# Performance work log

Measured on AMD Instinct MI355X. Metric: run time of the kernel, lower is better.

Reference implementation:

```python
import jax, jax.numpy as jnp
import numpy as np

D = 64            # node_out_feats
G = 1000          # number of graphs in batch
NPG = 32          # nodes per graph
N = G * NPG       # total nodes = 32000
E = 80000         # total edges
NODE_IN = 74
EDGE_IN = 12
EH = 128          # edge_hidden_feats
STEPS_MP = 6
STEPS_S2S = 6
LSTM_LAYERS = 3
N_TASKS = 1


def setup_inputs() -> dict:
    key = jax.random.key(0)
    ks = jax.random.split(key, 32)

    def lin(k, fi, fo):
        return (jax.random.normal(k, (fi, fo), jnp.float32) / np.float32(np.sqrt(fi)))

    # edges constrained within graphs
    eg = jax.random.randint(ks[0], (E,), 0, G)
    inp = {
        "node_feats": jax.random.normal(ks[1], (N, NODE_IN), jnp.float32),
        "edge_feats": jax.random.normal(ks[2], (E, EDGE_IN), jnp.float32),
        "src": (eg * NPG + jax.random.randint(ks[3], (E,), 0, NPG)).astype(jnp.int32),
        "dst": (eg * NPG + jax.random.randint(ks[4], (E,), 0, NPG)).astype(jnp.int32),
        "segment_ids": (jnp.arange(N, dtype=jnp.int32) // NPG),
        "Wp": lin(ks[5], NODE_IN, D), "bp": jnp.zeros((D,), jnp.float32),
        "We1": lin(ks[6], EDGE_IN, EH), "be1": jnp.zeros((EH,), jnp.float32),
        "We2": lin(ks[7], EH, D * D), "be2": jnp.zeros((D * D,), jnp.float32),
        "b_conv": jnp.zeros((D,), jnp.float32),
        "gru_Wx": lin(ks[8], D, 3 * D), "gru_Wh": lin(ks[9], D, 3 * D),
        "gru_bx": jnp.zeros((3 * D,), jnp.float32), "gru_bh": jnp.zeros((3 * D,), jnp.float32),
        "Wout1": lin(ks[10], 2 * D, D), "bout1": jnp.zeros((D,), jnp.float32),
        "Wout2": lin(ks[11], D, N_TASKS), "bout2": jnp.zeros((N_TASKS,), jnp.float32),
    }
    for l in range(LSTM_LAYERS):
        fi = 2 * D if l == 0 else D
        inp[f"lstm_Wx{l}"] = lin(ks[12 + 4 * l], fi, 4 * D)
        inp[f"lstm_Wh{l}"] = lin(ks[13 + 4 * l], D, 4 * D)
        inp[f"lstm_bx{l}"] = jnp.zeros((4 * D,), jnp.float32)
        inp[f"lstm_bh{l}"] = jnp.zeros((4 * D,), jnp.float32)
    return inp


def reference(node_feats, edge_feats, src, dst, segment_ids,
              Wp, bp, We1, be1, We2, be2, b_conv,
              gru_Wx, gru_Wh, gru_bx, gru_bh,
              Wout1, bout1, Wout2, bout2,
              lstm_Wx0, lstm_Wh0, lstm_bx0, lstm_bh0,
              lstm_Wx1, lstm_Wh1, lstm_bx1, lstm_bh1,
              lstm_Wx2, lstm_Wh2, lstm_bx2, lstm_bh2):
    # ---- MPNNGNN ----
    h = jax.nn.relu(node_feats @ Wp + bp)                 # [N, D]
    hidden = h                                            # GRU hidden state
    # edge network -> per-edge [D, D] weight matrix (edge feats are constant,
    # so compute once; DGL recomputes each step with identical result)
    W_edge = (jax.nn.relu(edge_feats @ We1 + be1) @ We2 + be2).reshape(E, D, D)
    for _ in range(STEPS_MP):
        msg = jnp.einsum('ed,edo->eo', h[src], W_edge)    # [E, D] per-edge matvec
        agg = jax.ops.segment_sum(msg, dst, num_segments=N) + b_conv
        x = jax.nn.relu(agg)
        # GRU cell (torch gate order r, z, n)
        gx = x @ gru_Wx + gru_bx
        gh = hidden @ gru_Wh + gru_bh
        r = jax.nn.sigmoid(gx[:, :D] + gh[:, :D])
        z = jax.nn.sigmoid(gx[:, D:2 * D] + gh[:, D:2 * D])
        n = jnp.tanh(gx[:, 2 * D:] + r * gh[:, 2 * D:])
        hidden = (1.0 - z) * n + z * hidden
        h = hidden
    # ---- Set2Set readout ----
    lstm = [(lstm_Wx0, lstm_Wh0, lstm_bx0, lstm_bh0),
            (lstm_Wx1, lstm_Wh1, lstm_bx1, lstm_bh1),
            (lstm_Wx2, lstm_Wh2, lstm_bx2, lstm_bh2)]
    hs = [jnp.zeros((G, D), h.dtype) for _ in range(LSTM_LAYERS)]
    cs = [jnp.zeros((G, D), h.dtype) for _ in range(LSTM_LAYERS)]
    q_star = jnp.zeros((G, 2 * D), h.dtype)
    for _ in range(STEPS_S2S):
        xq = q_star
        for l, (Wx, Wh, bx, bh) in enumerate(lstm):
            gates = xq @ Wx + bx + hs[l] @ Wh + bh        # [G, 4D], torch order i,f,g,o
            i, f, g_, o = jnp.split(gates, 4, axis=-1)
            c = jax.nn.sigmoid(f) * cs[l] + jax.nn.sigmoid(i) * jnp.tanh(g_)
            hs[l] = jax.nn.sigmoid(o) * jnp.tanh(c)
            cs[l] = c
            xq = hs[l]
        q = xq                                            # [G, D]
        e = jnp.sum(h * q[segment_ids], axis=-1)          # [N] attention logits
        emax = jax.ops.segment_max(e, segment_ids, num_segments=G)
        ee = jnp.exp(e - emax[segment_ids])
        alpha = ee / jax.ops.segment_sum(ee, segment_ids, num_segments=G)[segment_ids]
        readout = jax.ops.segment_sum(h * alpha[:, None], segment_ids, num_segments=G)
        q_star = jnp.concatenate([q, readout], axis=-1)   # [G, 2D]
    # ---- prediction head ----
    pred = jax.nn.relu(q_star @ Wout1 + bout1) @ Wout2 + bout2
    return pred, q_star
```

## Files before the change

### kernel.cpp

```cpp
#include <hip/hip_runtime.h>

typedef __attribute__((ext_vector_type(8))) _Float16 f16x8;
typedef __attribute__((ext_vector_type(4))) float floatx4;

union HFrag { uint4 u4; f16x8 v; unsigned short s[8]; };
union HS { _Float16 h; unsigned short u; };

__device__ __forceinline__ float bf2f(unsigned short u) {
  return __uint_as_float(((unsigned int)u) << 16);
}
__device__ __forceinline__ float h2f(unsigned short u) { HS z; z.u = u; return (float)z.h; }
__device__ __forceinline__ unsigned short f2h(float f) { HS z; z.h = (_Float16)f; return z.u; }
__device__ __forceinline__ float sigmf(float x) { return 1.0f / (1.0f + expf(-x)); }

__device__ __forceinline__ float ldi(const void* p, long i, bool f32) {
  return f32 ? ((const float*)p)[i] : bf2f(((const unsigned short*)p)[i]);
}

__device__ __forceinline__ void dma16(unsigned short* lds, const unsigned short* g) {
  __builtin_amdgcn_global_load_lds(
      (const __attribute__((address_space(1))) unsigned int*)g,
      (__attribute__((address_space(3))) unsigned int*)lds,
      16, 0, 0);
}

#define WAIT_VM8()   __builtin_amdgcn_s_waitcnt(0x0F78)
#define WAIT_VM4()   __builtin_amdgcn_s_waitcnt(0x0F74)
#define WAIT_VM0()   __builtin_amdgcn_s_waitcnt(0x0F70)
#define WAIT_LGKM0() __builtin_amdgcn_s_waitcnt(0xC07F)

#define NNODES 32000
#define NEDGES 80000
#define NGRAPH 1000

#define MFMA_F16 __builtin_amdgcn_mfma_f32_16x16x32_f16

__global__ __launch_bounds__(256) void detect_kernel(
    const unsigned short* __restrict__ nf, int* __restrict__ flag) {
  __shared__ float sm[256];
  float m = 0.f;
  for (int i = threadIdx.x; i < 4096; i += 256) {
    float v = fabsf(bf2f(nf[i]));
    if (isfinite(v)) m = fmaxf(m, v);
    else m = 1e30f;
  }
  sm[threadIdx.x] = m;
  __syncthreads();
  if (threadIdx.x == 0) {
    float mm = 0.f;
    for (int i = 0; i < 256; ++i) mm = fmaxf(mm, sm[i]);
    flag[0] = (mm > 1e6f) ? 1 : 0;
  }
}

__global__ __launch_bounds__(256) void prep_kernel(
    const int* __restrict__ dflag,
    const void* __restrict__ Wx, const void* __restrict__ Wh,
    const void* __restrict__ bx, const void* __restrict__ bh,
    const void* __restrict__ bconv,
    unsigned short* __restrict__ WxH, unsigned short* __restrict__ WhH,
    float* __restrict__ bxf, float* __restrict__ bhf, float* __restrict__ bconvf) {
  bool f32 = dflag[0] != 0;
  int idx = blockIdx.x * 256 + threadIdx.x;
  int j = idx >> 6, k = idx & 63;
  WxH[idx] = f2h(ldi(Wx, k * 192 + j, f32));
  WhH[idx] = f2h(ldi(Wh, k * 192 + j, f32));
  if (idx < 192) { bxf[idx] = ldi(bx, idx, f32); bhf[idx] = ldi(bh, idx, f32); }
  if (idx < 64) bconvf[idx] = ldi(bconv, idx, f32);
}

__global__ __launch_bounds__(256) void lstmprep_kernel(
    const int* __restrict__ dflag,
    const void* Wx0, const void* Wh0, const void* bx0, const void* bh0,
    const void* Wx1, const void* Wh1, const void* bx1, const void* bh1,
    const void* Wx2, const void* Wh2, const void* bx2, const void* bh2,
    float4* __restrict__ LW, float* __restrict__ bsum) {
  bool f32 = dflag[0] != 0;
  int idx = blockIdx.x * 256 + threadIdx.x;
  int l, base, fi;
  if (idx < 12288)      { l = 0; base = 0;     fi = 128; }
  else if (idx < 20480) { l = 1; base = 12288; fi = 64; }
  else                  { l = 2; base = 20480; fi = 64; }
  const void* Wx = (l == 0) ? Wx0 : (l == 1) ? Wx1 : Wx2;
  const void* Wh = (l == 0) ? Wh0 : (l == 1) ? Wh1 : Wh2;
  int r = idx - base;
  int c = r >> 8, t = r & 255;
  float v[4];
#pragma unroll
  for (int i2 = 0; i2 < 4; ++i2) {
    int k = c * 4 + i2;
    v[i2] = (k < fi) ? ldi(Wx, (long)k * 256 + t, f32)
                     : ldi(Wh, (long)(k - fi) * 256 + t, f32);
  }
  float4 o; o.x = v[0]; o.y = v[1]; o.z = v[2]; o.w = v[3];
  LW[idx] = o;
  if (idx < 768) {
    int ll = idx >> 8, j = idx & 255;
    const void* bx = (ll == 0) ? bx0 : (ll == 1) ? bx1 : bx2;
    const void* bh = (ll == 0) ? bh0 : (ll == 1) ? bh1 : bh2;
    bsum[idx] = ldi(bx, j, f32) + ldi(bh, j, f32);
  }
}

__global__ __launch_bounds__(256) void nodeproj_kernel(
    const int* __restrict__ dflag,
    const void* __restrict__ nf, const void* __restrict__ Wp,
    const void* __restrict__ bp, float* __restrict__ hstate) {
  bool f32 = dflag[0] != 0;
  int lane = threadIdx.x & 63;
  int n = blockIdx.x * 4 + (threadIdx.x >> 6);
  float acc = ldi(bp, lane, f32);
  for (int k = 0; k < 74; ++k)
    acc += ldi(nf, (long)n * 74 + k, f32) * ldi(Wp, k * 64 + lane, f32);
  hstate[n * 64 + lane] = fmaxf(acc, 0.0f);
}

__global__ __launch_bounds__(256) void we2h_kernel(
    const int* __restrict__ dflag,
    const void* __restrict__ We2, unsigned short* __restrict__ We2Hsw) {
  bool f32 = dflag[0] != 0;
  int idx = blockIdx.x * 256 + threadIdx.x;
  int j = idx & 7;
  int cc = (idx >> 3) & 15;
  int o = (idx >> 7) & 63;
  int d = idx >> 13;
  int k = ((cc ^ (o & 15)) << 3) | j;
  We2Hsw[idx] = f2h(ldi(We2, (long)k * 4096 + d * 64 + o, f32));
}

__global__ __launch_bounds__(256) void count_kernel(
    const int* __restrict__ dst, int* __restrict__ cnt) {
  int e = blockIdx.x * 256 + threadIdx.x;
  if (e < NEDGES) atomicAdd(&cnt[dst[e]], 1);
}

__global__ __launch_bounds__(256) void scan_kernel(
    const int* __restrict__ cnt, int* __restrict__ row_ptr, int* __restrict__ cur) {
  __shared__ int part[256];
  int t = threadIdx.x;
  int base = t * 125;
  int s = 0;
  for (int i = 0; i < 125; ++i) s += cnt[base + i];
  part[t] = s;
  __syncthreads();
  if (t == 0) {
    int run = 0;
    for (int i = 0; i < 256; ++i) { int v = part[i]; part[i] = run; run += v; }
  }
  __syncthreads();
  int run = part[t];
  for (int i = 0; i < 125; ++i) {
    row_ptr[base + i] = run;
    cur[base + i] = run;
    run += cnt[base + i];
  }
  if (t == 255) row_ptr[32000] = run;
}

__global__ __launch_bounds__(256) void fill_kernel(
    const int* __restrict__ dst, int* __restrict__ cur, int* __restrict__ eidx) {
  int e = blockIdx.x * 256 + threadIdx.x;
  if (e < NEDGES) { int p = atomicAdd(&cur[dst[e]], 1); eidx[p] = e; }
}

__global__ __launch_bounds__(256, 2) void msg_fused_kernel(
    const int* __restrict__ dflag,
    const float* __restrict__ hstate,
    const void* __restrict__ ef, const void* __restrict__ We1,
    const void* __restrict__ be1, const void* __restrict__ be2,
    const unsigned short* __restrict__ We2Hsw,
    const int* __restrict__ src, const int* __restrict__ eidx,
    float* __restrict__ msgbuf) {
  bool f32 = dflag[0] != 0;
  __shared__ __align__(16) unsigned short u_s[64][136];
  __shared__ float h_s[64][65];
  __shared__ __align__(8) unsigned short be2h[64][72];
  __shared__ int ssrc[64];
  __shared__ int seidx[64];
  __shared__ __align__(16) unsigned short wbuf[2][8192];
  float* ef_s = (float*)&wbuf[0][0];
  float* we1_s = (float*)&wbuf[0][2048];
  float* be1_s = (float*)&wbuf[1][0];

  int t = threadIdx.x;
  int e0 = blockIdx.x * 64;
  int lane = t & 63, w = t >> 6;

  if (t < 64) { int e = eidx[e0 + t]; seidx[t] = e; ssrc[t] = src[e]; }
  for (int i = t; i < 1536; i += 256) we1_s[i] = ldi(We1, i, f32);
  if (t < 128) be1_s[t] = ldi(be1, t, f32);
  for (int i = t; i < 4096; i += 256) be2h[i >> 6][i & 63] = f2h(ldi(be2, i, f32));
  __syncthreads();
  for (int i = t; i < 768; i += 256) {
    int slot = i / 12, k = i - slot * 12;
    ef_s[i] = ldi(ef, (long)seidx[slot] * 12 + k, f32);
  }
  __syncthreads();

#pragma unroll
  for (int i = 0; i < 32; ++i) {
    int idx = t + i * 256;
    int row = idx >> 7, col = idx & 127;
    float acc = be1_s[col];
#pragma unroll
    for (int k = 0; k < 12; ++k) acc += ef_s[row * 12 + k] * we1_s[k * 128 + col];
    u_s[row][col] = f2h(fmaxf(acc, 0.f));
  }
#pragma unroll
  for (int i = 0; i < 16; ++i) {
    int idx = t + i * 256;
    int row = idx >> 6, col = idx & 63;
    h_s[row][col] = hstate[(size_t)ssrc[row] * 64 + col];
  }
  __syncthreads();

  int o0 = w * 16;
  int c = lane & 15, q = lane >> 4;
  HFrag ub[4][4];
#pragma unroll
  for (int g = 0; g < 4; ++g)
#pragma unroll
    for (int kk = 0; kk < 4; ++kk)
      ub[g][kk].u4 = *(const uint4*)&u_s[g * 16 + c][q * 8 + kk * 32];
  floatx4 msg[4];
#pragma unroll
  for (int g = 0; g < 4; ++g) msg[g] = (floatx4){0.f, 0.f, 0.f, 0.f};
  int rowb = (o0 + c) * 16;

  unsigned short* buf0 = &wbuf[0][0];
  unsigned short* buf1 = &wbuf[1][0];
  unsigned short* buf2 = &u_s[0][0];

  {
    const unsigned short* g0 = We2Hsw + w * 2048 + lane * 8;
    unsigned short* l0 = buf0 + w * 2048;
    dma16(l0, g0); dma16(l0 + 512, g0 + 512);
    dma16(l0 + 1024, g0 + 1024); dma16(l0 + 1536, g0 + 1536);
    const unsigned short* g1 = g0 + 8192;
    unsigned short* l1 = buf1 + w * 2048;
    dma16(l1, g1); dma16(l1 + 512, g1 + 512);
    dma16(l1 + 1024, g1 + 1024); dma16(l1 + 1536, g1 + 1536);
  }
  __syncthreads();
  {
    const unsigned short* g2 = We2Hsw + 2 * 8192 + w * 2048 + lane * 8;
    unsigned short* l2 = buf2 + w * 2048;
    dma16(l2, g2); dma16(l2 + 512, g2 + 512);
    dma16(l2 + 1024, g2 + 1024); dma16(l2 + 1536, g2 + 1536);
  }

  int m3 = 0;
  for (int d = 0; d < 64; ++d) {
    if (d <= 61) WAIT_VM8();
    else if (d == 62) WAIT_VM4();
    else WAIT_VM0();
    unsigned short* wb = (m3 == 0) ? buf0 : (m3 == 1) ? buf1 : buf2;
    HFrag a0, a1, a2, a3;
    a0.u4 = *(const uint4*)&wb[(rowb + ((0 * 4 + q) ^ c)) * 8];
    a1.u4 = *(const uint4*)&wb[(rowb + ((1 * 4 + q) ^ c)) * 8];
    a2.u4 = *(const uint4*)&wb[(rowb + ((2 * 4 + q) ^ c)) * 8];
    a3.u4 = *(const uint4*)&wb[(rowb + ((3 * 4 + q) ^ c)) * 8];
    WAIT_LGKM0();
    if (d + 3 < 64) {
      const unsigned short* g = We2Hsw + (d + 3) * 8192 + w * 2048 + lane * 8;
      unsigned short* l = wb + w * 2048;
      dma16(l, g); dma16(l + 512, g + 512);
      dma16(l + 1024, g + 1024); dma16(l + 1536, g + 1536);
    }
    HS b0, b1, b2v, b3;
    const unsigned short* bp = &be2h[d][o0 + q * 4];
    b0.u = bp[0]; b1.u = bp[1]; b2v.u = bp[2]; b3.u = bp[3];
    float be0 = (float)b0.h, be1v = (float)b1.h, be2f = (float)b2v.h, be3 = (float)b3.h;
#pragma unroll
    for (int g = 0; g < 4; ++g) {
      floatx4 wv = {0.f, 0.f, 0.f, 0.f};
      wv = MFMA_F16(a0.v, ub[g][0].v, wv, 0, 0, 0);
      wv = MFMA_F16(a1.v, ub[g][1].v, wv, 0, 0, 0);
      wv = MFMA_F16(a2.v, ub[g][2].v, wv, 0, 0, 0);
      wv = MFMA_F16(a3.v, ub[g][3].v, wv, 0, 0, 0);
      float hv = h_s[g * 16 + c][d];
      msg[g][0] += hv * (wv[0] + be0);
      msg[g][1] += hv * (wv[1] + be1v);
      msg[g][2] += hv * (wv[2] + be2f);
      msg[g][3] += hv * (wv[3] + be3);
    }
    m3 = (m3 == 2) ? 0 : m3 + 1;
  }

#pragma unroll
  for (int g = 0; g < 4; ++g) {
    int slot = g * 16 + c;
    float4 st;
    st.x = msg[g][0]; st.y = msg[g][1]; st.z = msg[g][2]; st.w = msg[g][3];
    *(float4*)(msgbuf + (size_t)(e0 + slot) * 64 + o0 + q * 4) = st;
  }
}

__global__ __launch_bounds__(256, 2) void gru_kernel(
    float* __restrict__ hstate, const float* __restrict__ msgbuf,
    const int* __restrict__ row_ptr,
    const unsigned short* __restrict__ WxH, const unsigned short* __restrict__ WhH,
    const float* __restrict__ bxf, const float* __restrict__ bhf,
    const float* __restrict__ bconvf) {
  __shared__ __align__(16) unsigned short Xhi[64][72];
  __shared__ __align__(16) unsigned short Xlo[64][72];
  __shared__ __align__(16) unsigned short Hh[64][72];
  __shared__ unsigned short SRZ[128][68];
  __shared__ float GXn[64][66];
  __shared__ float GHn[64][66];
  int t = threadIdx.x;
  int nb = blockIdx.x * 64;

#pragma unroll
  for (int i = 0; i < 16; ++i) {
    int idx = t + i * 256;
    int n = idx >> 6, c = idx & 63;
    int node = nb + n;
    float a = bconvf[c];
    int p0 = row_ptr[node], p1 = row_ptr[node + 1];
    for (int p = p0; p < p1; ++p) a += msgbuf[(size_t)p * 64 + c];
    a = fmaxf(a, 0.f);
    HS hi; hi.h = (_Float16)a;
    Xhi[n][c] = hi.u;
    Xlo[n][c] = f2h(a - (float)hi.h);
    Hh[n][c] = f2h(hstate[(size_t)node * 64 + c]);
  }
  __syncthreads();

  int lane = t & 63, w = t >> 6;
  int c16 = lane & 15, q = lane >> 4;
  floatx4 gx[3][4], gh[3][4];
#pragma unroll
  for (int jt = 0; jt < 3; ++jt)
#pragma unroll
    for (int nt = 0; nt < 4; ++nt) {
      gx[jt][nt] = (floatx4){0.f, 0.f, 0.f, 0.f};
      gh[jt][nt] = (floatx4){0.f, 0.f, 0.f, 0.f};
    }
#pragma unroll
  for (int kc = 0; kc < 2; ++kc) {
    int kof = kc * 32 + q * 8;
    HFrag ax[3], ah[3];
#pragma unroll
    for (int jt = 0; jt < 3; ++jt) {
      long off = (long)((w * 3 + jt) * 16 + c16) * 64 + kof;
      ax[jt].u4 = *(const uint4*)(WxH + off);
      ah[jt].u4 = *(const uint4*)(WhH + off);
    }
    HFrag bxh[4], bxl[4], bhf_[4];
#pragma unroll
    for (int nt = 0; nt < 4; ++nt) {
      int n = nt * 16 + c16;
      bxh[nt].u4 = *(const uint4*)&Xhi[n][kof];
      bxl[nt].u4 = *(const uint4*)&Xlo[n][kof];
      bhf_[nt].u4 = *(const uint4*)&Hh[n][kof];
    }
#pragma unroll
    for (int jt = 0; jt < 3; ++jt)
#pragma unroll
      for (int nt = 0; nt < 4; ++nt) {
        gx[jt][nt] = MFMA_F16(ax[jt].v, bxh[nt].v, gx[jt][nt], 0, 0, 0);
        gx[jt][nt] = MFMA_F16(ax[jt].v, bxl[nt].v, gx[jt][nt], 0, 0, 0);
        gh[jt][nt] = MFMA_F16(ah[jt].v, bhf_[nt].v, gh[jt][nt], 0, 0, 0);
      }
  }

#pragma unroll
  for (int jt = 0; jt < 3; ++jt) {
#pragma unroll
    for (int rr = 0; rr < 4; ++rr) {
      int j = (w * 3 + jt) * 16 + q * 4 + rr;
      float bxv = bxf[j], bhv = bhf[j];
#pragma unroll
      for (int nt = 0; nt < 4; ++nt) {
        int n = nt * 16 + c16;
        float vx = gx[jt][nt][rr] + bxv;
        float vh = gh[jt][nt][rr] + bhv;
        if (j < 128) {
          SRZ[j][n] = f2h(sigmf(vx + vh));
        } else {
          GXn[j - 128][n] = vx;
          GHn[j - 128][n] = vh;
        }
      }
    }
  }
  __syncthreads();

#pragma unroll
  for (int i = 0; i < 16; ++i) {
    int idx = t + i * 256;
    int n = idx >> 6, f = idx & 63;
    float r = h2f(SRZ[f][n]);
    float z = h2f(SRZ[64 + f][n]);
    float ng = tanhf(GXn[f][n] + r * GHn[f][n]);
    size_t gi = (size_t)(nb + n) * 64 + f;
    float ho = hstate[gi];
    hstate[gi] = (1.0f - z) * ng + z * ho;
  }
}

__global__ __launch_bounds__(512) void s2s6_kernel(
    const int* __restrict__ dflag,
    const float* __restrict__ hstate,
    const float4* __restrict__ LW,
    const float* __restrict__ lstm_bsum,
    const void* __restrict__ Wout1, const void* __restrict__ bout1,
    const void* __restrict__ Wout2, const void* __restrict__ bout2,
    float* __restrict__ out) {
  bool f32 = dflag[0] != 0;
  __shared__ float xq[4][128];
  __shared__ float inb[4][192];
  __shared__ float gates[4][256];
  __shared__ float al[4][32];
  __shared__ float hsvf[768];
  __shared__ float csvf[768];
  int g0 = blockIdx.x * 4;
  int t = threadIdx.x;

  for (int i = t; i < 512; i += 512) xq[i >> 7][i & 127] = 0.f;
  for (int i = t; i < 768; i += 512) { hsvf[i] = 0.f; csvf[i] = 0.f; }
  __syncthreads();

  int tt = t & 255, gp = t >> 8;
  int ga = gp * 2, gb = ga + 1;

  for (int s = 0; s < 6; ++s) {
#pragma unroll
    for (int l = 0; l < 3; ++l) {
      const int fi = (l == 0) ? 128 : 64;
      const int tot = fi + 64;
      for (int i = t; i < 4 * tot; i += 512) {
        int g = i / tot, k = i - g * tot;
        inb[g][k] = (k < fi) ? xq[g][k] : hsvf[l * 256 + g * 64 + (k - fi)];
      }
      __syncthreads();
      const int nch = tot >> 2;
      const float4* wrow = LW + ((l == 0) ? 0 : (l == 1) ? 12288 : 20480) + tt;
      float bs = lstm_bsum[l * 256 + tt];
      float a0 = bs, a1 = bs;
#pragma unroll 8
      for (int cch = 0; cch < nch; ++cch) {
        float4 wv = wrow[(size_t)cch * 256];
        float4 x0 = *(const float4*)&inb[ga][cch * 4];
        float4 x1 = *(const float4*)&inb[gb][cch * 4];
        a0 += wv.x * x0.x + wv.y * x0.y + wv.z * x0.z + wv.w * x0.w;
        a1 += wv.x * x1.x + wv.y * x1.y + wv.z * x1.z + wv.w * x1.w;
      }
      gates[ga][tt] = a0;
      gates[gb][tt] = a1;
      __syncthreads();
      if (t < 256) {
        int gg = t >> 6, u = t & 63;
        float ig = sigmf(gates[gg][u]);
        float fg = sigmf(gates[gg][64 + u]);
        float gv = tanhf(gates[gg][128 + u]);
        float og = sigmf(gates[gg][192 + u]);
        int ci = l * 256 + t;
        float cc = fg * csvf[ci] + ig * gv;
        float hn = og * tanhf(cc);
        csvf[ci] = cc;
        hsvf[ci] = hn;
        xq[gg][u] = hn;
      }
      __syncthreads();
    }
    if (t < 256) {
      int gg = t >> 6, tl = t & 63;
      int g = g0 + gg;
      int n = tl & 31, half = tl >> 5;
      const float* hrow = hstate + (size_t)(g * 32 + n) * 64 + half * 32;
      const float* qp = &xq[gg][half * 32];
      float p = 0.f;
#pragma unroll
      for (int k = 0; k < 32; ++k) p += hrow[k] * qp[k];
      p += __shfl_xor(p, 32, 64);
      if (half == 0) {
        float m = p;
#pragma unroll
        for (int s2 = 1; s2 < 32; s2 <<= 1) m = fmaxf(m, __shfl_xor(m, s2, 32));
        float e = expf(p - m);
        float sum = e;
#pragma unroll
        for (int s2 = 1; s2 < 32; s2 <<= 1) sum += __shfl_xor(sum, s2, 32);
        al[gg][n] = e / sum;
      }
      float acc = 0.f;
#pragma unroll 8
      for (int nn = 0; nn < 32; ++nn)
        acc += al[gg][nn] * hstate[(size_t)(g * 32 + nn) * 64 + tl];
      xq[gg][64 + tl] = acc;
    }
    __syncthreads();
  }

  if (t < 256) {
    int gg = t >> 6, tl = t & 63;
    int g = g0 + gg;
    float acc = ldi(bout1, tl, f32);
#pragma unroll 16
    for (int k = 0; k < 128; ++k) acc += xq[gg][k] * ldi(Wout1, k * 64 + tl, f32);
    acc = fmaxf(acc, 0.0f);
    float p = acc * ldi(Wout2, tl, f32);
#pragma unroll
    for (int m = 1; m < 64; m <<= 1) p += __shfl_xor(p, m, 64);
    if (tl == 0) out[g] = p + ldi(bout2, 0, f32);
    out[1000 + g * 128 + tl] = xq[gg][tl];
    out[1000 + g * 128 + 64 + tl] = xq[gg][64 + tl];
  }
}

extern "C" void kernel_launch(void* const* d_in, const int* in_sizes, int n_in,
                              void* d_out, int out_size, void* d_ws, size_t ws_size,
                              hipStream_t stream) {
  (void)in_sizes; (void)n_in; (void)out_size; (void)ws_size;
  const void* node_feats = d_in[0];
  const void* edge_feats = d_in[1];
  const int* src = (const int*)d_in[2];
  const int* dst = (const int*)d_in[3];
  const void* Wp = d_in[5];
  const void* bp = d_in[6];
  const void* We1 = d_in[7];
  const void* be1 = d_in[8];
  const void* We2 = d_in[9];
  const void* be2 = d_in[10];
  const void* b_conv = d_in[11];
  const void* gWx = d_in[12];
  const void* gWh = d_in[13];
  const void* gbx = d_in[14];
  const void* gbh = d_in[15];
  const void* Wout1 = d_in[16];
  const void* bout1 = d_in[17];
  const void* Wout2 = d_in[18];
  const void* bout2 = d_in[19];

  int* dflag = (int*)d_ws;
  float* hstate = (float*)d_ws + 64;
  float* msgbuf = hstate + NNODES * 64;
  unsigned short* We2Hsw = (unsigned short*)(msgbuf + (size_t)NEDGES * 64);
  unsigned short* WxH = We2Hsw + 524288;
  unsigned short* WhH = WxH + 12288;
  float* bxf = (float*)(WhH + 12288);
  float* bhf = bxf + 192;
  float* bconvf = bhf + 192;
  int* row_ptr = (int*)(bconvf + 64);
  int* cur = row_ptr + 32001;
  int* cnt = cur + 32000;
  int* eidx = cnt + 32000;
  uintptr_t lwp = (uintptr_t)(eidx + 80000);
  lwp = (lwp + 15) & ~(uintptr_t)15;
  float4* LWf = (float4*)lwp;
  float* lstm_bsum = (float*)(LWf + 28672);

  (void)hipMemsetAsync(cnt, 0, (size_t)NNODES * sizeof(int), stream);

  detect_kernel<<<1, 256, 0, stream>>>((const unsigned short*)node_feats, dflag);
  prep_kernel<<<48, 256, 0, stream>>>(dflag, gWx, gWh, gbx, gbh, b_conv,
                                      WxH, WhH, bxf, bhf, bconvf);
  nodeproj_kernel<<<NNODES / 4, 256, 0, stream>>>(dflag, node_feats, Wp, bp, hstate);
  we2h_kernel<<<2048, 256, 0, stream>>>(dflag, We2, We2Hsw);
  lstmprep_kernel<<<112, 256, 0, stream>>>(dflag,
      d_in[20], d_in[21], d_in[22], d_in[23],
      d_in[24], d_in[25], d_in[26], d_in[27],
      d_in[28], d_in[29], d_in[30], d_in[31],
      LWf, lstm_bsum);

  count_kernel<<<(NEDGES + 255) / 256, 256, 0, stream>>>(dst, cnt);
  scan_kernel<<<1, 256, 0, stream>>>(cnt, row_ptr, cur);
  fill_kernel<<<(NEDGES + 255) / 256, 256, 0, stream>>>(dst, cur, eidx);

  for (int step = 0; step < 6; ++step) {
    msg_fused_kernel<<<NEDGES / 64, 256, 0, stream>>>(
        dflag, hstate, edge_feats, We1, be1, be2, We2Hsw, src, eidx, msgbuf);
    gru_kernel<<<NNODES / 64, 256, 0, stream>>>(hstate, msgbuf, row_ptr,
                                                WxH, WhH, bxf, bhf, bconvf);
  }
  s2s6_kernel<<<NGRAPH / 4, 512, 0, stream>>>(dflag, hstate,
      (const float4*)LWf, lstm_bsum,
      Wout1, bout1, Wout2, bout2, (float*)d_out);
}
```

Before: 1.274 ms.

## Reassociate edge network: precompute per-node h·We2 products, combine with edge hidden

The per-edge 64x64 weight matrix is no longer built. Each block now takes a 64-node destination tile and computes Z = h·We2 for every hidden unit k on its source nodes, with h split into fp16 hi and lo parts so the tensor-core products keep precision. Each edge's message is then accumulated as a sum over k of u_k times Z[src,k]. This cuts the large GEMM from scaling with edges to scaling with nodes. In exchange it adds doubled MFMAs for the hi/lo split, many block barriers per k-chunk, and heavy LDS use that limits occupancy. It also assumes every edge's source lies in the same 64-node tile as its destination.

```diff
diff --git a/kernel.cpp b/kernel.cpp
--- a/kernel.cpp
+++ b/kernel.cpp
@@ -28,6 +28,13 @@
 #define WAIT_VM4()   __builtin_amdgcn_s_waitcnt(0x0F74)
 #define WAIT_VM0()   __builtin_amdgcn_s_waitcnt(0x0F70)
 #define WAIT_LGKM0() __builtin_amdgcn_s_waitcnt(0xC07F)
+
+#define SAFE_BARRIER() do {                      \
+  __builtin_amdgcn_sched_barrier(0);             \
+  WAIT_LGKM0();                                  \
+  __builtin_amdgcn_s_barrier();                  \
+  __builtin_amdgcn_sched_barrier(0);             \
+} while (0)
 
 #define NNODES 32000
 #define NEDGES 80000
@@ -115,17 +122,33 @@
   hstate[n * 64 + lane] = fmaxf(acc, 0.0f);
 }
 
-__global__ __launch_bounds__(256) void we2h_kernel(
+__global__ __launch_bounds__(256) void we2t_kernel(
     const int* __restrict__ dflag,
-    const void* __restrict__ We2, unsigned short* __restrict__ We2Hsw) {
+    const void* __restrict__ We2, unsigned short* __restrict__ We2T) {
   bool f32 = dflag[0] != 0;
   int idx = blockIdx.x * 256 + threadIdx.x;
   int j = idx & 7;
-  int cc = (idx >> 3) & 15;
-  int o = (idx >> 7) & 63;
-  int d = idx >> 13;
-  int k = ((cc ^ (o & 15)) << 3) | j;
-  We2Hsw[idx] = f2h(ldi(We2, (long)k * 4096 + d * 64 + o, f32));
+  int gs = (idx >> 3) & 7;
+  int row = (idx >> 6) & 127;
+  int kc = idx >> 13;
+  int g = gs ^ (row & 7);
+  int d = g * 8 + j;
+  int o = row & 63;
+  int k = kc * 2 + (row >> 6);
+  We2T[idx] = f2h(ldi(We2, (long)k * 4096 + d * 64 + o, f32));
+}
+
+__global__ __launch_bounds__(256) void be2t_kernel(
+    const int* __restrict__ dflag,
+    const void* __restrict__ be2, unsigned short* __restrict__ be2T) {
+  bool f32 = dflag[0] != 0;
+  int idx = blockIdx.x * 256 + threadIdx.x;
+  int j = idx & 7;
+  int gs = (idx >> 3) & 7;
+  int o = idx >> 6;
+  int g = gs ^ (o & 7);
+  int d = g * 8 + j;
+  be2T[idx] = f2h(ldi(be2, (long)d * 64 + o, f32));
 }
 
 __global__ __launch_bounds__(256) void count_kernel(
@@ -163,136 +186,186 @@
   if (e < NEDGES) { int p = atomicAdd(&cur[dst[e]], 1); eidx[p] = e; }
 }
 
-__global__ __launch_bounds__(256, 2) void msg_fused_kernel(
+__global__ __launch_bounds__(256) void msg_z_kernel(
     const int* __restrict__ dflag,
     const float* __restrict__ hstate,
     const void* __restrict__ ef, const void* __restrict__ We1,
-    const void* __restrict__ be1, const void* __restrict__ be2,
-    const unsigned short* __restrict__ We2Hsw,
+    const void* __restrict__ be1,
+    const unsigned short* __restrict__ We2T,
+    const unsigned short* __restrict__ be2T,
     const int* __restrict__ src, const int* __restrict__ eidx,
+    const int* __restrict__ row_ptr,
     float* __restrict__ msgbuf) {
   bool f32 = dflag[0] != 0;
-  __shared__ __align__(16) unsigned short u_s[64][136];
-  __shared__ float h_s[64][65];
-  __shared__ __align__(8) unsigned short be2h[64][72];
-  __shared__ int ssrc[64];
-  __shared__ int seidx[64];
-  __shared__ __align__(16) unsigned short wbuf[2][8192];
-  float* ef_s = (float*)&wbuf[0][0];
-  float* we1_s = (float*)&wbuf[0][2048];
-  float* be1_s = (float*)&wbuf[1][0];
-
-  int t = threadIdx.x;
-  int e0 = blockIdx.x * 64;
-  int lane = t & 63, w = t >> 6;
-
-  if (t < 64) { int e = eidx[e0 + t]; seidx[t] = e; ssrc[t] = src[e]; }
+  __shared__ __align__(16) unsigned short hhi[64][72];
+  __shared__ __align__(16) unsigned short hlo[64][72];
+  __shared__ __align__(16) unsigned short BtL[2][8192];
+  __shared__ __align__(16) float Zs[8192];
+  __shared__ __align__(16) unsigned short beT[4096];
+  __shared__ float we1_s[1536];
+  __shared__ float be1_s[128];
+
+  int t = threadIdx.x, lane = t & 63, w = t >> 6;
+  int c = lane & 15, q = lane >> 4;
+  int nb = blockIdx.x * 64;
+  int p0 = row_ptr[nb], p1 = row_ptr[nb + 64];
+  int nE = p1 - p0;
+  if (nE <= 0) return;
+
+  for (int i = t; i < 4096; i += 256) {
+    int n = i >> 6, cc = i & 63;
+    float v = hstate[(size_t)(nb + n) * 64 + cc];
+    HS hi; hi.h = (_Float16)v;
+    hhi[n][cc] = hi.u;
+    hlo[n][cc] = f2h(v - (float)hi.h);
+  }
   for (int i = t; i < 1536; i += 256) we1_s[i] = ldi(We1, i, f32);
   if (t < 128) be1_s[t] = ldi(be1, t, f32);
-  for (int i = t; i < 4096; i += 256) be2h[i >> 6][i & 63] = f2h(ldi(be2, i, f32));
-  __syncthreads();
-  for (int i = t; i < 768; i += 256) {
-    int slot = i / 12, k = i - slot * 12;
-    ef_s[i] = ldi(ef, (long)seidx[slot] * 12 + k, f32);
-  }
-  __syncthreads();
-
-#pragma unroll
-  for (int i = 0; i < 32; ++i) {
-    int idx = t + i * 256;
-    int row = idx >> 7, col = idx & 127;
-    float acc = be1_s[col];
-#pragma unroll
-    for (int k = 0; k < 12; ++k) acc += ef_s[row * 12 + k] * we1_s[k * 128 + col];
-    u_s[row][col] = f2h(fmaxf(acc, 0.f));
-  }
-#pragma unroll
-  for (int i = 0; i < 16; ++i) {
-    int idx = t + i * 256;
-    int row = idx >> 6, col = idx & 63;
-    h_s[row][col] = hstate[(size_t)ssrc[row] * 64 + col];
-  }
-  __syncthreads();
-
-  int o0 = w * 16;
-  int c = lane & 15, q = lane >> 4;
-  HFrag ub[4][4];
-#pragma unroll
-  for (int g = 0; g < 4; ++g)
-#pragma unroll
-    for (int kk = 0; kk < 4; ++kk)
-      ub[g][kk].u4 = *(const uint4*)&u_s[g * 16 + c][q * 8 + kk * 32];
-  floatx4 msg[4];
-#pragma unroll
-  for (int g = 0; g < 4; ++g) msg[g] = (floatx4){0.f, 0.f, 0.f, 0.f};
-  int rowb = (o0 + c) * 16;
-
-  unsigned short* buf0 = &wbuf[0][0];
-  unsigned short* buf1 = &wbuf[1][0];
-  unsigned short* buf2 = &u_s[0][0];
-
-  {
-    const unsigned short* g0 = We2Hsw + w * 2048 + lane * 8;
-    unsigned short* l0 = buf0 + w * 2048;
-    dma16(l0, g0); dma16(l0 + 512, g0 + 512);
-    dma16(l0 + 1024, g0 + 1024); dma16(l0 + 1536, g0 + 1536);
-    const unsigned short* g1 = g0 + 8192;
-    unsigned short* l1 = buf1 + w * 2048;
-    dma16(l1, g1); dma16(l1 + 512, g1 + 512);
-    dma16(l1 + 1024, g1 + 1024); dma16(l1 + 1536, g1 + 1536);
-  }
-  __syncthreads();
-  {
-    const unsigned short* g2 = We2Hsw + 2 * 8192 + w * 2048 + lane * 8;
-    unsigned short* l2 = buf2 + w * 2048;
-    dma16(l2, g2); dma16(l2 + 512, g2 + 512);
-    dma16(l2 + 1024, g2 + 1024); dma16(l2 + 1536, g2 + 1536);
-  }
-
-  int m3 = 0;
-  for (int d = 0; d < 64; ++d) {
-    if (d <= 61) WAIT_VM8();
-    else if (d == 62) WAIT_VM4();
-    else WAIT_VM0();
-    unsigned short* wb = (m3 == 0) ? buf0 : (m3 == 1) ? buf1 : buf2;
-    HFrag a0, a1, a2, a3;
-    a0.u4 = *(const uint4*)&wb[(rowb + ((0 * 4 + q) ^ c)) * 8];
-    a1.u4 = *(const uint4*)&wb[(rowb + ((1 * 4 + q) ^ c)) * 8];
-    a2.u4 = *(const uint4*)&wb[(rowb + ((2 * 4 + q) ^ c)) * 8];
-    a3.u4 = *(const uint4*)&wb[(rowb + ((3 * 4 + q) ^ c)) * 8];
-    WAIT_LGKM0();
-    if (d + 3 < 64) {
-      const unsigned short* g = We2Hsw + (d + 3) * 8192 + w * 2048 + lane * 8;
-      unsigned short* l = wb + w * 2048;
-      dma16(l, g); dma16(l + 512, g + 512);
-      dma16(l + 1024, g + 1024); dma16(l + 1536, g + 1536);
-    }
-    HS b0, b1, b2v, b3;
-    const unsigned short* bp = &be2h[d][o0 + q * 4];
-    b0.u = bp[0]; b1.u = bp[1]; b2v.u = bp[2]; b3.u = bp[3];
-    float be0 = (float)b0.h, be1v = (float)b1.h, be2f = (float)b2v.h, be3 = (float)b3.h;
-#pragma unroll
-    for (int g = 0; g < 4; ++g) {
-      floatx4 wv = {0.f, 0.f, 0.f, 0.f};
-      wv = MFMA_F16(a0.v, ub[g][0].v, wv, 0, 0, 0);
-      wv = MFMA_F16(a1.v, ub[g][1].v, wv, 0, 0, 0);
-      wv = MFMA_F16(a2.v, ub[g][2].v, wv, 0, 0, 0);
-      wv = MFMA_F16(a3.v, ub[g][3].v, wv, 0, 0, 0);
-      float hv = h_s[g * 16 + c][d];
-      msg[g][0] += hv * (wv[0] + be0);
-      msg[g][1] += hv * (wv[1] + be1v);
-      msg[g][2] += hv * (wv[2] + be2f);
-      msg[g][3] += hv * (wv[3] + be3);
-    }
-    m3 = (m3 == 2) ? 0 : m3 + 1;
-  }
-
-#pragma unroll
-  for (int g = 0; g < 4; ++g) {
-    int slot = g * 16 + c;
-    float4 st;
-    st.x = msg[g][0]; st.y = msg[g][1]; st.z = msg[g][2]; st.w = msg[g][3];
-    *(float4*)(msgbuf + (size_t)(e0 + slot) * 64 + o0 + q * 4) = st;
+  dma16(beT + w * 1024, be2T + w * 1024 + lane * 8);
+  dma16(beT + w * 1024 + 512, be2T + w * 1024 + 512 + lane * 8);
+  SAFE_BARRIER();
+
+  for (int et = 0; et < nE; et += 256) {
+    int me = et + t;
+    bool act = me < nE;
+    int pos = p0 + (act ? me : 0);
+    int eg = eidx[pos];
+    int r = src[eg] - nb;
+    float efr[12];
+#pragma unroll
+    for (int j = 0; j < 12; ++j) efr[j] = ldi(ef, (long)eg * 12 + j, f32);
+
+#pragma unroll
+    for (int b = 0; b < 2; ++b) {
+      unsigned short* L = &BtL[b][0];
+      const unsigned short* G = We2T + b * 8192;
+      int o1 = w * 1024, o2 = 4096 + w * 1024;
+      dma16(L + o1, G + o1 + lane * 8);
+      dma16(L + o1 + 512, G + o1 + 512 + lane * 8);
+      dma16(L + o2, G + o2 + lane * 8);
+      dma16(L + o2 + 512, G + o2 + 512 + lane * 8);
+    }
+    WAIT_VM8();
+
+    floatx4 hacc[4];
+#pragma unroll
+    for (int mt = 0; mt < 4; ++mt) hacc[mt] = (floatx4){0.f, 0.f, 0.f, 0.f};
+#pragma unroll
+    for (int ks = 0; ks < 2; ++ks) {
+      HFrag bb;
+      bb.u4 = *(const uint4*)&beT[(w * 16 + c) * 64 + (((ks * 4 + q) ^ (c & 7)) * 8)];
+#pragma unroll
+      for (int mt = 0; mt < 4; ++mt) {
+        HFrag ah, al;
+        ah.u4 = *(const uint4*)&hhi[mt * 16 + c][ks * 32 + q * 8];
+        al.u4 = *(const uint4*)&hlo[mt * 16 + c][ks * 32 + q * 8];
+        hacc[mt] = MFMA_F16(ah.v, bb.v, hacc[mt], 0, 0, 0);
+        hacc[mt] = MFMA_F16(al.v, bb.v, hacc[mt], 0, 0, 0);
+      }
+    }
+    SAFE_BARRIER();
+#pragma unroll
+    for (int mt = 0; mt < 4; ++mt) {
+#pragma unroll
+      for (int reg = 0; reg < 4; ++reg) {
+        int row = mt * 16 + q * 4 + reg;
+        int col = w * 16 + c;
+        int gp = (col >> 2) ^ (row & 15);
+        Zs[row * 128 + gp * 4 + (col & 3)] = hacc[mt][reg];
+      }
+    }
+    SAFE_BARRIER();
+
+    floatx4 msgv[16];
+    int rb = r * 128, rx = r & 15;
+    if (act) {
+#pragma unroll
+      for (int og = 0; og < 16; ++og)
+        msgv[og] = *(const floatx4*)&Zs[rb + (og ^ rx) * 4];
+    }
+
+    for (int kc = 0; kc < 64; ++kc) {
+      if (kc == 63) WAIT_VM0(); else WAIT_VM4();
+      HFrag bf[2][2];
+#pragma unroll
+      for (int nt2 = 0; nt2 < 2; ++nt2)
+#pragma unroll
+        for (int ks = 0; ks < 2; ++ks) {
+          int row = (nt2 * 4 + w) * 16 + c;
+          int gq = (ks * 4 + q) ^ (c & 7);
+          bf[nt2][ks].u4 = *(const uint4*)&BtL[kc & 1][row * 64 + gq * 8];
+        }
+      __builtin_amdgcn_sched_barrier(0);
+      WAIT_LGKM0();
+      __builtin_amdgcn_sched_barrier(0);
+      if (kc + 2 < 64) {
+        unsigned short* L = &BtL[kc & 1][0];
+        const unsigned short* G = We2T + (kc + 2) * 8192;
+        int o1 = w * 1024, o2 = 4096 + w * 1024;
+        dma16(L + o1, G + o1 + lane * 8);
+        dma16(L + o1 + 512, G + o1 + 512 + lane * 8);
+        dma16(L + o2, G + o2 + lane * 8);
+        dma16(L + o2 + 512, G + o2 + 512 + lane * 8);
+      }
+      floatx4 zacc[4][2];
+#pragma unroll
+      for (int mt = 0; mt < 4; ++mt)
+#pragma unroll
+        for (int nt2 = 0; nt2 < 2; ++nt2)
+          zacc[mt][nt2] = (floatx4){0.f, 0.f, 0.f, 0.f};
+#pragma unroll
+      for (int ks = 0; ks < 2; ++ks) {
+#pragma unroll
+        for (int mt = 0; mt < 4; ++mt) {
+          HFrag ah, al;
+          ah.u4 = *(const uint4*)&hhi[mt * 16 + c][ks * 32 + q * 8];
+          al.u4 = *(const uint4*)&hlo[mt * 16 + c][ks * 32 + q * 8];
+#pragma unroll
+          for (int nt2 = 0; nt2 < 2; ++nt2) {
+            zacc[mt][nt2] = MFMA_F16(ah.v, bf[nt2][ks].v, zacc[mt][nt2], 0, 0, 0);
+            zacc[mt][nt2] = MFMA_F16(al.v, bf[nt2][ks].v, zacc[mt][nt2], 0, 0, 0);
+          }
+        }
+      }
+      SAFE_BARRIER();
+#pragma unroll
+      for (int mt = 0; mt < 4; ++mt)
+#pragma unroll
+        for (int nt2 = 0; nt2 < 2; ++nt2) {
+          int ntile = nt2 * 4 + w;
+#pragma unroll
+          for (int reg = 0; reg < 4; ++reg) {
+            int row = mt * 16 + q * 4 + reg;
+            int col = ntile * 16 + c;
+            int gp = (col >> 2) ^ (row & 15);
+            Zs[row * 128 + gp * 4 + (col & 3)] = zacc[mt][nt2][reg];
+          }
+        }
+      SAFE_BARRIER();
+
+      if (act) {
+        int k0 = kc * 2;
+        float u0 = be1_s[k0], u1 = be1_s[k0 + 1];
+#pragma unroll
+        for (int j = 0; j < 12; ++j) {
+          u0 += efr[j] * we1_s[j * 128 + k0];
+          u1 += efr[j] * we1_s[j * 128 + k0 + 1];
+        }
+        u0 = fmaxf(u0, 0.f); u1 = fmaxf(u1, 0.f);
+#pragma unroll
+        for (int og = 0; og < 16; ++og) {
+          floatx4 z0 = *(const floatx4*)&Zs[rb + (og ^ rx) * 4];
+          floatx4 z1 = *(const floatx4*)&Zs[rb + (16 + (og ^ rx)) * 4];
+          msgv[og] += u0 * z0 + u1 * z1;
+        }
+      }
+    }
+
+    if (act) {
+      float* mp = msgbuf + (size_t)pos * 64;
+#pragma unroll
+      for (int og = 0; og < 16; ++og) *(floatx4*)(mp + og * 4) = msgv[og];
+    }
   }
 }
 
@@ -537,8 +610,8 @@
   int* dflag = (int*)d_ws;
   float* hstate = (float*)d_ws + 64;
   float* msgbuf = hstate + NNODES * 64;
-  unsigned short* We2Hsw = (unsigned short*)(msgbuf + (size_t)NEDGES * 64);
-  unsigned short* WxH = We2Hsw + 524288;
+  unsigned short* We2T = (unsigned short*)(msgbuf + (size_t)NEDGES * 64);
+  unsigned short* WxH = We2T + 524288;
   unsigned short* WhH = WxH + 12288;
   float* bxf = (float*)(WhH + 12288);
   float* bhf = bxf + 192;
@@ -551,6 +624,7 @@
   lwp = (lwp + 15) & ~(uintptr_t)15;
   float4* LWf = (float4*)lwp;
   float* lstm_bsum = (float*)(LWf + 28672);
+  unsigned short* be2T = (unsigned short*)(lstm_bsum + 768);
 
   (void)hipMemsetAsync(cnt, 0, (size_t)NNODES * sizeof(int), stream);
 
@@ -558,7 +632,8 @@
   prep_kernel<<<48, 256, 0, stream>>>(dflag, gWx, gWh, gbx, gbh, b_conv,
                                       WxH, WhH, bxf, bhf, bconvf);
   nodeproj_kernel<<<NNODES / 4, 256, 0, stream>>>(dflag, node_feats, Wp, bp, hstate);
-  we2h_kernel<<<2048, 256, 0, stream>>>(dflag, We2, We2Hsw);
+  we2t_kernel<<<2048, 256, 0, stream>>>(dflag, We2, We2T);
+  be2t_kernel<<<16, 256, 0, stream>>>(dflag, be2, be2T);
   lstmprep_kernel<<<112, 256, 0, stream>>>(dflag,
       d_in[20], d_in[21], d_in[22], d_in[23],
       d_in[24], d_in[25], d_in[26], d_in[27],
@@ -570,8 +645,9 @@
   fill_kernel<<<(NEDGES + 255) / 256, 256, 0, stream>>>(dst, cur, eidx);
 
   for (int step = 0; step < 6; ++step) {
-    msg_fused_kernel<<<NEDGES / 64, 256, 0, stream>>>(
-        dflag, hstate, edge_feats, We1, be1, be2, We2Hsw, src, eidx, msgbuf);
+    msg_z_kernel<<<NNODES / 64, 256, 0, stream>>>(
+        dflag, hstate, edge_feats, We1, be1, We2T, be2T, src, eidx, row_ptr,
+        msgbuf);
     gru_kernel<<<NNODES / 64, 256, 0, stream>>>(hstate, msgbuf, row_ptr,
                                                 WxH, WhH, bxf, bhf, bconvf);
   }
```

Result: slower. 1.980 ms (+55.4%).
